# Kernel tuning notes

Hardware: AMD Instinct MI355X
Metric: run time of the kernel (lower is better)

The kernel has to match this reference:

```python
import jax, jax.numpy as jnp
import numpy as np

N = 30000   # nodes
E = 150000  # edges per graph
IN = 512
HID = 512
OUT = 256
G = 3


def setup_inputs() -> dict:
    key = jax.random.key(0)
    ks = jax.random.split(key, 16)
    inp = {"x": jax.random.normal(ks[0], (N, IN), jnp.float32)}
    for i in range(G):
        inp[f"edges{i}"] = jax.random.randint(ks[1 + i], (2, E), 0, N)
        inp[f"W{i}"] = jax.random.normal(ks[4 + i], (IN, HID), jnp.float32) / np.sqrt(IN)
        inp[f"b{i}"] = jnp.zeros((HID,), jnp.float32)
    inp["alphas"] = jnp.ones((G,), jnp.float32)
    inp["W_lin"] = jax.random.normal(ks[8], (HID * G, OUT), jnp.float32) / np.sqrt(HID * G)
    inp["b_lin"] = jnp.zeros((OUT,), jnp.float32)
    return inp


def graph_conv(edges, x, W, b):
    # DGL GraphConv, norm='both': out = D_in^{-1/2} A D_out^{-1/2} (X W) + b
    src, dst = edges[0], edges[1]
    ones = jnp.ones(edges.shape[1], x.dtype)
    deg_out = jnp.clip(jax.ops.segment_sum(ones, src, num_segments=N), 1.0)  # out-degree of src nodes
    deg_in = jnp.clip(jax.ops.segment_sum(ones, dst, num_segments=N), 1.0)   # in-degree of dst nodes
    h = (x * jax.lax.rsqrt(deg_out)[:, None]) @ W        # [N, HID] mult-W-first (in_dim >= hid_dim)
    agg = jax.ops.segment_sum(h[src], dst, num_segments=N)  # SpMM via gather + scatter-add
    return agg * jax.lax.rsqrt(deg_in)[:, None] + b


def reference(x, edges0, edges1, edges2, W0, W1, W2, b0, b1, b2, alphas, W_lin, b_lin):
    a = jax.nn.softmax(alphas)  # softmax over the n_graphs axis
    branches = [(edges0, W0, b0), (edges1, W1, b1), (edges2, W2, b2)]
    hs = [jnp.tanh(a[i] * graph_conv(e, x, W, b)) for i, (e, W, b) in enumerate(branches)]
    h = jnp.concatenate(hs, axis=1)  # [N, G*HID]; dropout(p=0) is identity
    return h @ W_lin + b_lin
```

## Files before the change

### kernel.cpp

```cpp
#include <hip/hip_runtime.h>

#define NN 30000
#define NE 150000
#define KIN 512
#define KHID 512
#define KOUT 256
#define NG 3
#define KCAT (KHID*NG)
#define MTILES ((NN + 127) / 128)
#define NCHUNK 30

typedef __attribute__((ext_vector_type(8))) __bf16 bf16x8;
typedef __attribute__((ext_vector_type(4))) float  f32x4;
typedef __attribute__((ext_vector_type(8))) unsigned short u16x8;

__device__ __forceinline__ unsigned short f2bf(float f) {
    unsigned u = __float_as_uint(f);
    u = (u + 0x7FFFu + ((u >> 16) & 1u)) >> 16;
    return (unsigned short)u;
}
__device__ __forceinline__ float bf2f(unsigned short u) {
    return __uint_as_float((unsigned)u << 16);
}
__device__ __forceinline__ float fast_tanh(float x) {
    float e = __expf(2.f * x);
    return 1.f - __fdividef(2.f, e + 1.f);
}
__device__ __forceinline__ void gl_lds16(const void* g, void* l) {
    __builtin_amdgcn_global_load_lds(
        (const __attribute__((address_space(1))) void*)g,
        (__attribute__((address_space(3))) void*)l, 16, 0, 0);
}

__global__ void k_count(const int* __restrict__ e0, const int* __restrict__ e1,
                        const int* __restrict__ e2, int* cnt_out, int* cnt_in) {
    int idx = blockIdx.x * 256 + threadIdx.x;
    if (idx >= NG * NE) return;
    int g = idx / NE, e = idx - g * NE;
    const int* ed = (g == 0) ? e0 : ((g == 1) ? e1 : e2);
    atomicAdd(&cnt_out[g * NN + ed[e]], 1);
    atomicAdd(&cnt_in [g * NN + ed[NE + e]], 1);
}

__global__ void k_rs(const int* cnt_out, const int* cnt_in, float* rs_out, float* rs_in) {
    int idx = blockIdx.x * 256 + threadIdx.x;
    if (idx >= NG * NN) return;
    int co = cnt_out[idx]; if (co < 1) co = 1;
    int ci = cnt_in [idx]; if (ci < 1) ci = 1;
    rs_out[idx] = rsqrtf((float)co);
    rs_in [idx] = rsqrtf((float)ci);
}

__global__ __launch_bounds__(256) void k_scan1(const int* __restrict__ cnt_in,
                                               int* __restrict__ csum) {
    int g = blockIdx.y, c = blockIdx.x;
    const int* cc = cnt_in + g * NN;
    int i = c * 1024 + threadIdx.x * 4;
    int4 v = {0, 0, 0, 0};
    if (i + 3 < NN) v = *(const int4*)(cc + i);
    else {
        if (i     < NN) v.x = cc[i];
        if (i + 1 < NN) v.y = cc[i + 1];
        if (i + 2 < NN) v.z = cc[i + 2];
        if (i + 3 < NN) v.w = cc[i + 3];
    }
    int s = v.x + v.y + v.z + v.w;
    #pragma unroll
    for (int o = 32; o > 0; o >>= 1) s += __shfl_down(s, o, 64);
    __shared__ int ws[4];
    if ((threadIdx.x & 63) == 0) ws[threadIdx.x >> 6] = s;
    __syncthreads();
    if (threadIdx.x == 0) csum[g * 32 + c] = ws[0] + ws[1] + ws[2] + ws[3];
}

__global__ void k_scan2(int* __restrict__ csum) {
    int g = threadIdx.x >> 6, lane = threadIdx.x & 63;
    if (g >= NG) return;
    int v = (lane < NCHUNK) ? csum[g * 32 + lane] : 0;
    int inc = v;
    #pragma unroll
    for (int o = 1; o < 32; o <<= 1) {
        int n = __shfl_up(inc, o, 64);
        if (lane >= o) inc += n;
    }
    if (lane < NCHUNK) csum[g * 32 + lane] = inc - v;
}

__global__ __launch_bounds__(256) void k_scan3(const int* __restrict__ cnt_in,
        const int* __restrict__ csum, int* __restrict__ row_off) {
    int g = blockIdx.y, c = blockIdx.x;
    const int* cc = cnt_in + g * NN;
    int* ro = row_off + g * (NN + 1);
    int tid = threadIdx.x, lane = tid & 63, w = tid >> 6;
    int i = c * 1024 + tid * 4;
    int4 v = {0, 0, 0, 0};
    if (i + 3 < NN) v = *(const int4*)(cc + i);
    else {
        if (i     < NN) v.x = cc[i];
        if (i + 1 < NN) v.y = cc[i + 1];
        if (i + 2 < NN) v.z = cc[i + 2];
        if (i + 3 < NN) v.w = cc[i + 3];
    }
    int s = v.x + v.y + v.z + v.w;
    int inc = s;
    #pragma unroll
    for (int o = 1; o < 64; o <<= 1) {
        int n = __shfl_up(inc, o, 64);
        if (lane >= o) inc += n;
    }
    __shared__ int ws[4];
    if (lane == 63) ws[w] = inc;
    __syncthreads();
    int base = csum[g * 32 + c];
    for (int k = 0; k < w; k++) base += ws[k];
    int excl = base + inc - s;
    if (i     < NN) ro[i]     = excl;
    if (i + 1 < NN) ro[i + 1] = excl + v.x;
    if (i + 2 < NN) ro[i + 2] = excl + v.x + v.y;
    if (i + 3 < NN) ro[i + 3] = excl + v.x + v.y + v.z;
    if (c == 0 && tid == 0) ro[NN] = NE;
}

__global__ void k_fill(const int* __restrict__ e0, const int* __restrict__ e1,
                       const int* __restrict__ e2, const int* __restrict__ row_off,
                       int* cursor, int* __restrict__ csr) {
    int idx = blockIdx.x * 256 + threadIdx.x;
    if (idx >= NG * NE) return;
    int g = idx / NE, e = idx - g * NE;
    const int* ed = (g == 0) ? e0 : ((g == 1) ? e1 : e2);
    int s = ed[e], d = ed[NE + e];
    int pos = atomicAdd(&cursor[g * NN + d], 1);
    csr[g * NE + row_off[g * (NN + 1) + d] + pos] = s;
}

__global__ void k_misc(const float* __restrict__ alphas,
                       const float* __restrict__ b0, const float* __restrict__ b1,
                       const float* __restrict__ b2, float* __restrict__ aptr,
                       float* __restrict__ bcat) {
    int idx = blockIdx.x * 256 + threadIdx.x;
    if (idx < NG * KHID) {
        int g = idx >> 9;
        const float* b = (g == 0) ? b0 : ((g == 1) ? b1 : b2);
        bcat[idx] = b[idx & 511];
    }
    if (idx == 0) {
        float m = fmaxf(alphas[0], fmaxf(alphas[1], alphas[2]));
        float ex0 = expf(alphas[0] - m), ex1 = expf(alphas[1] - m), ex2 = expf(alphas[2] - m);
        float s = ex0 + ex1 + ex2;
        aptr[0] = ex0 / s; aptr[1] = ex1 / s; aptr[2] = ex2 / s;
    }
}

__global__ __launch_bounds__(256) void k_wt(const float* __restrict__ W0,
        const float* __restrict__ W1, const float* __restrict__ W2,
        const float* __restrict__ Wlin,
        unsigned short* __restrict__ Wt, unsigned short* __restrict__ Wlt) {
    __shared__ float Ls[32][33];
    int bid = blockIdx.x;
    const float* src; unsigned short* dst; int ncols, kdim, k0, n0;
    if (bid < NG * 256) {
        int g = bid >> 8, t = bid & 255;
        int kt = t >> 4, nt = t & 15;
        src = (g == 0) ? W0 : ((g == 1) ? W1 : W2);
        dst = Wt + (size_t)g * KIN * KHID;
        ncols = KHID; kdim = KIN; k0 = kt * 32; n0 = nt * 32;
    } else {
        int t = bid - NG * 256;
        int kt = t % 48, nt = t / 48;
        src = Wlin; dst = Wlt; ncols = KOUT; kdim = KCAT; k0 = kt * 32; n0 = nt * 32;
    }
    int tid = threadIdx.x;
    int r = tid >> 3, c4 = (tid & 7) * 4;
    float4 v = *(const float4*)(src + (size_t)(k0 + r) * ncols + n0 + c4);
    Ls[r][c4 + 0] = v.x; Ls[r][c4 + 1] = v.y; Ls[r][c4 + 2] = v.z; Ls[r][c4 + 3] = v.w;
    __syncthreads();
    int nr = tid >> 3, kc = (tid & 7) * 4;
    ushort4 o;
    o.x = f2bf(Ls[kc + 0][nr]); o.y = f2bf(Ls[kc + 1][nr]);
    o.z = f2bf(Ls[kc + 2][nr]); o.w = f2bf(Ls[kc + 3][nr]);
    *(ushort4*)(dst + (size_t)(n0 + nr) * kdim + k0 + kc) = o;
}

__global__ void k_xbf(const float* __restrict__ x, unsigned short* __restrict__ xb) {
    size_t i = ((size_t)blockIdx.x * 256 + threadIdx.x) * 8;
    float4 v0 = *(const float4*)(x + i);
    float4 v1 = *(const float4*)(x + i + 4);
    uint4 pk;
    pk.x = (unsigned)f2bf(v0.x) | ((unsigned)f2bf(v0.y) << 16);
    pk.y = (unsigned)f2bf(v0.z) | ((unsigned)f2bf(v0.w) << 16);
    pk.z = (unsigned)f2bf(v1.x) | ((unsigned)f2bf(v1.y) << 16);
    pk.w = (unsigned)f2bf(v1.z) | ((unsigned)f2bf(v1.w) << 16);
    *(uint4*)(xb + i) = pk;
}

__global__ __launch_bounds__(256) void k_agg_bf(const unsigned short* __restrict__ xb,
        const int* __restrict__ csr, const int* __restrict__ row_off,
        const float* __restrict__ rs_out, const float* __restrict__ rs_in,
        unsigned short* __restrict__ y, size_t ystride, int gbase) {
    int g    = gbase + blockIdx.z;
    int d    = blockIdx.x * 4 + (threadIdx.x >> 6);
    int lane = threadIdx.x & 63;
    int beg = row_off[g * (NN + 1) + d];
    int end = row_off[g * (NN + 1) + d + 1];
    const int* cs = csr + g * NE;
    const float* rso = rs_out + g * NN;
    float a0=0,a1=0,a2=0,a3=0,a4=0,a5=0,a6=0,a7=0;
    const unsigned short* xbl = xb + lane * 8;
    int e = beg;
    for (; e + 1 < end; e += 2) {
        int s0 = cs[e], s1 = cs[e + 1];
        float w0 = rso[s0], w1 = rso[s1];
        u16x8 v0 = *(const u16x8*)(xbl + (size_t)s0 * KIN);
        u16x8 v1 = *(const u16x8*)(xbl + (size_t)s1 * KIN);
        a0 += w0 * bf2f(v0[0]) + w1 * bf2f(v1[0]);
        a1 += w0 * bf2f(v0[1]) + w1 * bf2f(v1[1]);
        a2 += w0 * bf2f(v0[2]) + w1 * bf2f(v1[2]);
        a3 += w0 * bf2f(v0[3]) + w1 * bf2f(v1[3]);
        a4 += w0 * bf2f(v0[4]) + w1 * bf2f(v1[4]);
        a5 += w0 * bf2f(v0[5]) + w1 * bf2f(v1[5]);
        a6 += w0 * bf2f(v0[6]) + w1 * bf2f(v1[6]);
        a7 += w0 * bf2f(v0[7]) + w1 * bf2f(v1[7]);
    }
    if (e < end) {
        int s0 = cs[e];
        float w0 = rso[s0];
        u16x8 v0 = *(const u16x8*)(xbl + (size_t)s0 * KIN);
        a0 += w0 * bf2f(v0[0]); a1 += w0 * bf2f(v0[1]);
        a2 += w0 * bf2f(v0[2]); a3 += w0 * bf2f(v0[3]);
        a4 += w0 * bf2f(v0[4]); a5 += w0 * bf2f(v0[5]);
        a6 += w0 * bf2f(v0[6]); a7 += w0 * bf2f(v0[7]);
    }
    float ri = rs_in[g * NN + d];
    uint4 pk;
    pk.x = (unsigned)f2bf(a0 * ri) | ((unsigned)f2bf(a1 * ri) << 16);
    pk.y = (unsigned)f2bf(a2 * ri) | ((unsigned)f2bf(a3 * ri) << 16);
    pk.z = (unsigned)f2bf(a4 * ri) | ((unsigned)f2bf(a5 * ri) << 16);
    pk.w = (unsigned)f2bf(a6 * ri) | ((unsigned)f2bf(a7 * ri) << 16);
    *(uint4*)(y + (size_t)g * ystride + (size_t)d * KIN + lane * 8) = pk;
}

__global__ __launch_bounds__(256) void k_agg_f32(const float* __restrict__ x,
        const int* __restrict__ csr, const int* __restrict__ row_off,
        const float* __restrict__ rs_out, const float* __restrict__ rs_in,
        unsigned short* __restrict__ y, int g) {
    int d    = blockIdx.x * 4 + (threadIdx.x >> 6);
    int lane = threadIdx.x & 63;
    int beg = row_off[g * (NN + 1) + d];
    int end = row_off[g * (NN + 1) + d + 1];
    const int* cs = csr + g * NE;
    float a0=0,a1=0,a2=0,a3=0,a4=0,a5=0,a6=0,a7=0;
    const float* xb = x + lane * 8;
    for (int e = beg; e < end; e++) {
        int s = cs[e];
        float wsc = rs_out[g * NN + s];
        const float4* xr = (const float4*)(xb + (size_t)s * KIN);
        float4 v0 = xr[0], v1 = xr[1];
        a0 += wsc * v0.x; a1 += wsc * v0.y; a2 += wsc * v0.z; a3 += wsc * v0.w;
        a4 += wsc * v1.x; a5 += wsc * v1.y; a6 += wsc * v1.z; a7 += wsc * v1.w;
    }
    float ri = rs_in[g * NN + d];
    uint4 pk;
    pk.x = (unsigned)f2bf(a0 * ri) | ((unsigned)f2bf(a1 * ri) << 16);
    pk.y = (unsigned)f2bf(a2 * ri) | ((unsigned)f2bf(a3 * ri) << 16);
    pk.z = (unsigned)f2bf(a4 * ri) | ((unsigned)f2bf(a5 * ri) << 16);
    pk.w = (unsigned)f2bf(a6 * ri) | ((unsigned)f2bf(a7 * ri) << 16);
    *(uint4*)(y + (size_t)d * KIN + lane * 8) = pk;
}

template<int KDIM, int BN, bool TANH>
__global__ __launch_bounds__(BN, 2) void k_gemm(const unsigned short* __restrict__ A,
        size_t agstride, const unsigned short* __restrict__ Bt,
        const float* __restrict__ bias, const float* __restrict__ aptr, int gbase,
        unsigned short* __restrict__ Tout, float* __restrict__ Fout) {
    constexpr int THREADS = BN;
    constexpr int NITER = KDIM / 32;
    constexpr int ACH = 512 / THREADS;
    constexpr int BCH = 4;
    __shared__ __align__(16) unsigned short As[2][128 * 32];
    __shared__ __align__(16) unsigned short Bs[2][BN * 32];
    int g = gbase + blockIdx.z;
    const unsigned short* Ab = A + (size_t)g * agstride;
    const unsigned short* Bb = TANH ? (Bt + (size_t)g * KIN * KHID) : Bt;
    const float* bb = TANH ? (bias + g * KHID) : bias;
    int m0 = blockIdx.x * 128;
    int tid = threadIdx.x, lane = tid & 63, w = tid >> 6;
    int mq = w & 1, nq = w >> 1;

    f32x4 acc[4][8];
    #pragma unroll
    for (int i = 0; i < 4; i++)
        #pragma unroll
        for (int j = 0; j < 8; j++) acc[i][j] = (f32x4){0.f, 0.f, 0.f, 0.f};

    const unsigned short* Ag[ACH];
    unsigned short* Al[ACH];
    #pragma unroll
    for (int j = 0; j < ACH; j++) {
        int c = tid + THREADS * j;
        int r = c >> 2, q = (c & 3) ^ ((c >> 3) & 3);
        int grow = m0 + r; if (grow >= NN) grow = NN - 1;
        Ag[j] = Ab + (size_t)grow * KDIM + q * 8;
        Al[j] = (unsigned short*)&As[0][c * 8];
    }
    const unsigned short* Bg[BCH];
    unsigned short* Bl[BCH];
    #pragma unroll
    for (int j = 0; j < BCH; j++) {
        int c = tid + THREADS * j;
        int r = c >> 2, q = (c & 3) ^ ((c >> 3) & 3);
        Bg[j] = Bb + (size_t)r * KDIM + q * 8;
        Bl[j] = (unsigned short*)&Bs[0][c * 8];
    }
    constexpr int ABUF = 128 * 32, BBUF = BN * 32;

    auto stage = [&](int buf, int k0) {
        #pragma unroll
        for (int j = 0; j < ACH; j++) gl_lds16(Ag[j] + k0, Al[j] + buf * ABUF);
        #pragma unroll
        for (int j = 0; j < BCH; j++) gl_lds16(Bg[j] + k0, Bl[j] + buf * BBUF);
    };

    int kqs = (((lane >> 4) ^ ((lane >> 1) & 3))) * 8;
    int arow = mq * 64 + (lane & 15);
    int nrow = nq * 128 + (lane & 15);

    stage(0, 0);
    for (int it = 0; it < NITER; it++) {
        __syncthreads();
        if (it + 1 < NITER) stage((it + 1) & 1, (it + 1) * 32);
        const unsigned short* Alb = As[it & 1];
        const unsigned short* Blb = Bs[it & 1];
        bf16x8 af[4], bfr[8];
        #pragma unroll
        for (int mi = 0; mi < 4; mi++) af[mi] = *(const bf16x8*)&Alb[(arow + mi * 16) * 32 + kqs];
        #pragma unroll
        for (int ni = 0; ni < 8; ni++) bfr[ni] = *(const bf16x8*)&Blb[(nrow + ni * 16) * 32 + kqs];
        #pragma unroll
        for (int mi = 0; mi < 4; mi++)
            #pragma unroll
            for (int ni = 0; ni < 8; ni++)
                acc[mi][ni] = __builtin_amdgcn_mfma_f32_16x16x32_bf16(af[mi], bfr[ni], acc[mi][ni], 0, 0, 0);
    }

    float ascale = TANH ? aptr[g] : 0.f;
    int rb = mq * 64 + (lane >> 4) * 4;
    #pragma unroll
    for (int mi = 0; mi < 4; mi++) {
        #pragma unroll
        for (int r = 0; r < 4; r++) {
            int row = m0 + rb + mi * 16 + r;
            if (row < NN) {
                #pragma unroll
                for (int ni = 0; ni < 8; ni++) {
                    int col = nq * 128 + ni * 16 + (lane & 15);
                    float v = acc[mi][ni][r] + bb[col];
                    if (TANH) {
                        Tout[(size_t)row * KCAT + g * KHID + col] = f2bf(fast_tanh(ascale * v));
                    } else {
                        Fout[(size_t)row * KOUT + col] = v;
                    }
                }
            }
        }
    }
}

extern "C" void kernel_launch(void* const* d_in, const int* in_sizes, int n_in,
                              void* d_out, int out_size, void* d_ws, size_t ws_size,
                              hipStream_t stream) {
    const float* x      = (const float*)d_in[0];
    const int*   e0     = (const int*)  d_in[1];
    const float* W0     = (const float*)d_in[2];
    const float* b0     = (const float*)d_in[3];
    const int*   e1     = (const int*)  d_in[4];
    const float* W1     = (const float*)d_in[5];
    const float* b1     = (const float*)d_in[6];
    const int*   e2     = (const int*)  d_in[7];
    const float* W2     = (const float*)d_in[8];
    const float* b2     = (const float*)d_in[9];
    const float* alphas = (const float*)d_in[10];
    const float* Wlin   = (const float*)d_in[11];
    const float* blin   = (const float*)d_in[12];
    float* out = (float*)d_out;

    char* ws = (char*)d_ws;
    size_t off = 0;
    auto alloc = [&](size_t bytes) -> void* {
        void* p = ws + off;
        off = (off + bytes + 255) & ~(size_t)255;
        return p;
    };
    int*   cnt_out = (int*)  alloc((size_t)NG * NN * 4);
    int*   cnt_in  = (int*)  alloc((size_t)NG * NN * 4);
    int*   cursor  = (int*)  alloc((size_t)NG * NN * 4);
    int*   row_off = (int*)  alloc((size_t)NG * (NN + 1) * 4);
    int*   csr     = (int*)  alloc((size_t)NG * NE * 4);
    int*   csum    = (int*)  alloc((size_t)NG * 32 * 4);
    float* rs_out  = (float*)alloc((size_t)NG * NN * 4);
    float* rs_in   = (float*)alloc((size_t)NG * NN * 4);
    float* aptr    = (float*)alloc(16);
    float* bcat    = (float*)alloc((size_t)NG * KHID * 4);
    unsigned short* Wt  = (unsigned short*)alloc((size_t)NG * KIN * KHID * 2);
    unsigned short* Wlt = (unsigned short*)alloc((size_t)KCAT * KOUT * 2);

    const size_t SZ_Y1 = (size_t)NN * KIN * 2;
    const size_t SZ_T  = (size_t)NN * KCAT * 2;
    size_t remaining = (ws_size > off) ? (ws_size - off) : 0;
    int mode;
    if      (remaining >= 3 * SZ_Y1 + SZ_T + 8192)          mode = 2;
    else if (remaining >= SZ_Y1 + SZ_Y1 + SZ_T + 8192)      mode = 1;
    else                                                    mode = 0;

    unsigned short *y, *xb, *t;
    if (mode == 2) {
        y  = (unsigned short*)alloc(3 * SZ_Y1);
        t  = (unsigned short*)alloc(SZ_T);
        xb = t;
    } else if (mode == 1) {
        y  = (unsigned short*)alloc(SZ_Y1);
        xb = (unsigned short*)alloc(SZ_Y1);
        t  = (unsigned short*)alloc(SZ_T);
    } else {
        y  = (unsigned short*)alloc(SZ_Y1);
        xb = nullptr;
        t  = (unsigned short*)alloc(SZ_T);
    }

    hipMemsetAsync(cnt_out, 0, (size_t)((char*)cursor - (char*)cnt_out) + (size_t)NG * NN * 4, stream);

    k_count<<<(NG * NE + 255) / 256, 256, 0, stream>>>(e0, e1, e2, cnt_out, cnt_in);
    k_rs<<<(NG * NN + 255) / 256, 256, 0, stream>>>(cnt_out, cnt_in, rs_out, rs_in);
    k_scan1<<<dim3(NCHUNK, NG), 256, 0, stream>>>(cnt_in, csum);
    k_scan2<<<1, 192, 0, stream>>>(csum);
    k_scan3<<<dim3(NCHUNK, NG), 256, 0, stream>>>(cnt_in, csum, row_off);
    k_fill<<<(NG * NE + 255) / 256, 256, 0, stream>>>(e0, e1, e2, row_off, cursor, csr);
    k_misc<<<(NG * KHID + 255) / 256, 256, 0, stream>>>(alphas, b0, b1, b2, aptr, bcat);
    k_wt<<<NG * 256 + 384, 256, 0, stream>>>(W0, W1, W2, Wlin, Wt, Wlt);

    if (mode >= 1) {
        k_xbf<<<NN * KIN / (256 * 8), 256, 0, stream>>>(x, xb);
    }

    if (mode == 2) {
        k_agg_bf<<<dim3(NN / 4, 1, NG), 256, 0, stream>>>(
            xb, csr, row_off, rs_out, rs_in, y, (size_t)NN * KIN, 0);
        k_gemm<KIN, 512, true><<<dim3(MTILES, 1, NG), 512, 0, stream>>>(
            y, (size_t)NN * KIN, Wt, bcat, aptr, 0, t, nullptr);
    } else {
        for (int g = 0; g < NG; g++) {
            if (mode == 1)
                k_agg_bf<<<dim3(NN / 4, 1, 1), 256, 0, stream>>>(
                    xb, csr, row_off, rs_out, rs_in, y, 0, g);
            else
                k_agg_f32<<<NN / 4, 256, 0, stream>>>(x, csr, row_off, rs_out, rs_in, y, g);
            k_gemm<KIN, 512, true><<<dim3(MTILES, 1, 1), 512, 0, stream>>>(
                y, 0, Wt, bcat, aptr, g, t, nullptr);
        }
    }
    k_gemm<KCAT, 256, false><<<dim3(MTILES, 1, 1), 256, 0, stream>>>(
        t, 0, Wlt, blin, nullptr, 0, nullptr, out);
}
```

Measured before the change: 422.0 us.

## Retile GEMMs to 256-thread blocks with N-tiling and unroll aggregation by four

After: 405.5 us. 3.9% less time.

```diff
diff --git a/kernel.cpp b/kernel.cpp
--- a/kernel.cpp
+++ b/kernel.cpp
@@ -8,6 +8,7 @@
 #define NG 3
 #define KCAT (KHID*NG)
 #define MTILES ((NN + 127) / 128)
+#define MT64   ((NN + 63) / 64)
 #define NCHUNK 30
 
 typedef __attribute__((ext_vector_type(8))) __bf16 bf16x8;
@@ -207,21 +208,23 @@
     float a0=0,a1=0,a2=0,a3=0,a4=0,a5=0,a6=0,a7=0;
     const unsigned short* xbl = xb + lane * 8;
     int e = beg;
-    for (; e + 1 < end; e += 2) {
-        int s0 = cs[e], s1 = cs[e + 1];
-        float w0 = rso[s0], w1 = rso[s1];
+    for (; e + 3 < end; e += 4) {
+        int s0 = cs[e], s1 = cs[e+1], s2 = cs[e+2], s3 = cs[e+3];
+        float w0 = rso[s0], w1 = rso[s1], w2 = rso[s2], w3 = rso[s3];
         u16x8 v0 = *(const u16x8*)(xbl + (size_t)s0 * KIN);
         u16x8 v1 = *(const u16x8*)(xbl + (size_t)s1 * KIN);
-        a0 += w0 * bf2f(v0[0]) + w1 * bf2f(v1[0]);
-        a1 += w0 * bf2f(v0[1]) + w1 * bf2f(v1[1]);
-        a2 += w0 * bf2f(v0[2]) + w1 * bf2f(v1[2]);
-        a3 += w0 * bf2f(v0[3]) + w1 * bf2f(v1[3]);
-        a4 += w0 * bf2f(v0[4]) + w1 * bf2f(v1[4]);
-        a5 += w0 * bf2f(v0[5]) + w1 * bf2f(v1[5]);
-        a6 += w0 * bf2f(v0[6]) + w1 * bf2f(v1[6]);
-        a7 += w0 * bf2f(v0[7]) + w1 * bf2f(v1[7]);
-    }
-    if (e < end) {
+        u16x8 v2 = *(const u16x8*)(xbl + (size_t)s2 * KIN);
+        u16x8 v3 = *(const u16x8*)(xbl + (size_t)s3 * KIN);
+        a0 += w0*bf2f(v0[0]) + w1*bf2f(v1[0]) + w2*bf2f(v2[0]) + w3*bf2f(v3[0]);
+        a1 += w0*bf2f(v0[1]) + w1*bf2f(v1[1]) + w2*bf2f(v2[1]) + w3*bf2f(v3[1]);
+        a2 += w0*bf2f(v0[2]) + w1*bf2f(v1[2]) + w2*bf2f(v2[2]) + w3*bf2f(v3[2]);
+        a3 += w0*bf2f(v0[3]) + w1*bf2f(v1[3]) + w2*bf2f(v2[3]) + w3*bf2f(v3[3]);
+        a4 += w0*bf2f(v0[4]) + w1*bf2f(v1[4]) + w2*bf2f(v2[4]) + w3*bf2f(v3[4]);
+        a5 += w0*bf2f(v0[5]) + w1*bf2f(v1[5]) + w2*bf2f(v2[5]) + w3*bf2f(v3[5]);
+        a6 += w0*bf2f(v0[6]) + w1*bf2f(v1[6]) + w2*bf2f(v2[6]) + w3*bf2f(v3[6]);
+        a7 += w0*bf2f(v0[7]) + w1*bf2f(v1[7]) + w2*bf2f(v2[7]) + w3*bf2f(v3[7]);
+    }
+    for (; e < end; e++) {
         int s0 = cs[e];
         float w0 = rso[s0];
         u16x8 v0 = *(const u16x8*)(xbl + (size_t)s0 * KIN);
@@ -267,36 +270,37 @@
     *(uint4*)(y + (size_t)d * KIN + lane * 8) = pk;
 }
 
-template<int KDIM, int BN, bool TANH>
-__global__ __launch_bounds__(BN, 2) void k_gemm(const unsigned short* __restrict__ A,
+template<int KDIM, int BM, int BN, bool TANH>
+__global__ __launch_bounds__(256) void k_gemm(const unsigned short* __restrict__ A,
         size_t agstride, const unsigned short* __restrict__ Bt,
         const float* __restrict__ bias, const float* __restrict__ aptr, int gbase,
         unsigned short* __restrict__ Tout, float* __restrict__ Fout) {
-    constexpr int THREADS = BN;
     constexpr int NITER = KDIM / 32;
-    constexpr int ACH = 512 / THREADS;
-    constexpr int BCH = 4;
-    __shared__ __align__(16) unsigned short As[2][128 * 32];
+    constexpr int ACH = BM * 4 / 256;
+    constexpr int BCH = BN * 4 / 256;
+    constexpr int MQ = BM / 64;
+    __shared__ __align__(16) unsigned short As[2][BM * 32];
     __shared__ __align__(16) unsigned short Bs[2][BN * 32];
     int g = gbase + blockIdx.z;
     const unsigned short* Ab = A + (size_t)g * agstride;
-    const unsigned short* Bb = TANH ? (Bt + (size_t)g * KIN * KHID) : Bt;
+    const unsigned short* Bb = (TANH ? (Bt + (size_t)g * KIN * KHID) : Bt);
     const float* bb = TANH ? (bias + g * KHID) : bias;
-    int m0 = blockIdx.x * 128;
+    int m0 = blockIdx.y * BM;
+    int n0 = blockIdx.x * BN;
     int tid = threadIdx.x, lane = tid & 63, w = tid >> 6;
-    int mq = w & 1, nq = w >> 1;
-
-    f32x4 acc[4][8];
+    int mq = w % MQ, nq = w / MQ;
+
+    f32x4 acc[4][4];
     #pragma unroll
     for (int i = 0; i < 4; i++)
         #pragma unroll
-        for (int j = 0; j < 8; j++) acc[i][j] = (f32x4){0.f, 0.f, 0.f, 0.f};
+        for (int j = 0; j < 4; j++) acc[i][j] = (f32x4){0.f, 0.f, 0.f, 0.f};
 
     const unsigned short* Ag[ACH];
     unsigned short* Al[ACH];
     #pragma unroll
     for (int j = 0; j < ACH; j++) {
-        int c = tid + THREADS * j;
+        int c = tid + 256 * j;
         int r = c >> 2, q = (c & 3) ^ ((c >> 3) & 3);
         int grow = m0 + r; if (grow >= NN) grow = NN - 1;
         Ag[j] = Ab + (size_t)grow * KDIM + q * 8;
@@ -306,12 +310,12 @@
     unsigned short* Bl[BCH];
     #pragma unroll
     for (int j = 0; j < BCH; j++) {
-        int c = tid + THREADS * j;
+        int c = tid + 256 * j;
         int r = c >> 2, q = (c & 3) ^ ((c >> 3) & 3);
-        Bg[j] = Bb + (size_t)r * KDIM + q * 8;
+        Bg[j] = Bb + (size_t)(n0 + r) * KDIM + q * 8;
         Bl[j] = (unsigned short*)&Bs[0][c * 8];
     }
-    constexpr int ABUF = 128 * 32, BBUF = BN * 32;
+    constexpr int ABUF = BM * 32, BBUF = BN * 32;
 
     auto stage = [&](int buf, int k0) {
         #pragma unroll
@@ -322,7 +326,7 @@
 
     int kqs = (((lane >> 4) ^ ((lane >> 1) & 3))) * 8;
     int arow = mq * 64 + (lane & 15);
-    int nrow = nq * 128 + (lane & 15);
+    int nrow = nq * 64 + (lane & 15);
 
     stage(0, 0);
     for (int it = 0; it < NITER; it++) {
@@ -330,15 +334,15 @@
         if (it + 1 < NITER) stage((it + 1) & 1, (it + 1) * 32);
         const unsigned short* Alb = As[it & 1];
         const unsigned short* Blb = Bs[it & 1];
-        bf16x8 af[4], bfr[8];
+        bf16x8 af[4], bfr[4];
         #pragma unroll
         for (int mi = 0; mi < 4; mi++) af[mi] = *(const bf16x8*)&Alb[(arow + mi * 16) * 32 + kqs];
         #pragma unroll
-        for (int ni = 0; ni < 8; ni++) bfr[ni] = *(const bf16x8*)&Blb[(nrow + ni * 16) * 32 + kqs];
+        for (int ni = 0; ni < 4; ni++) bfr[ni] = *(const bf16x8*)&Blb[(nrow + ni * 16) * 32 + kqs];
         #pragma unroll
         for (int mi = 0; mi < 4; mi++)
             #pragma unroll
-            for (int ni = 0; ni < 8; ni++)
+            for (int ni = 0; ni < 4; ni++)
                 acc[mi][ni] = __builtin_amdgcn_mfma_f32_16x16x32_bf16(af[mi], bfr[ni], acc[mi][ni], 0, 0, 0);
     }
 
@@ -351,8 +355,8 @@
             int row = m0 + rb + mi * 16 + r;
             if (row < NN) {
                 #pragma unroll
-                for (int ni = 0; ni < 8; ni++) {
-                    int col = nq * 128 + ni * 16 + (lane & 15);
+                for (int ni = 0; ni < 4; ni++) {
+                    int col = n0 + nq * 64 + ni * 16 + (lane & 15);
                     float v = acc[mi][ni][r] + bb[col];
                     if (TANH) {
                         Tout[(size_t)row * KCAT + g * KHID + col] = f2bf(fast_tanh(ascale * v));
@@ -444,7 +448,7 @@
     if (mode == 2) {
         k_agg_bf<<<dim3(NN / 4, 1, NG), 256, 0, stream>>>(
             xb, csr, row_off, rs_out, rs_in, y, (size_t)NN * KIN, 0);
-        k_gemm<KIN, 512, true><<<dim3(MTILES, 1, NG), 512, 0, stream>>>(
+        k_gemm<KIN, 128, 128, true><<<dim3(KHID / 128, MTILES, NG), 256, 0, stream>>>(
             y, (size_t)NN * KIN, Wt, bcat, aptr, 0, t, nullptr);
     } else {
         for (int g = 0; g < NG; g++) {
@@ -453,10 +457,10 @@
                     xb, csr, row_off, rs_out, rs_in, y, 0, g);
             else
                 k_agg_f32<<<NN / 4, 256, 0, stream>>>(x, csr, row_off, rs_out, rs_in, y, g);
-            k_gemm<KIN, 512, true><<<dim3(MTILES, 1, 1), 512, 0, stream>>>(
+            k_gemm<KIN, 128, 128, true><<<dim3(KHID / 128, MTILES, 1), 256, 0, stream>>>(
                 y, 0, Wt, bcat, aptr, g, t, nullptr);
         }
     }
-    k_gemm<KCAT, 256, false><<<dim3(MTILES, 1, 1), 256, 0, stream>>>(
+    k_gemm<KCAT, 64, 256, false><<<dim3(1, MT64, 1), 256, 0, stream>>>(
         t, 0, Wlt, blin, nullptr, 0, nullptr, out);
 }
```
